# Kernel tuning notes

Hardware: AMD Instinct MI355X
Metric: run time of the kernel (lower is better)

## Reference

```python
import jax, jax.numpy as jnp
import numpy as np

N, E, B = 65536, 262144, 2048   # nodes, edges, graphs
ND, ED, H, L = 32, 8, 128, 4    # node feat, edge feat, hidden, egnn layers
PE, PH, CH = 1280, 512, 512     # protein embed, protein hidden, combined hidden
EPS = 1e-8


def _seg_mean(data, ids, num):
    s = jax.ops.segment_sum(data, ids, num_segments=num)
    c = jax.ops.segment_sum(jnp.ones((data.shape[0], 1), data.dtype), ids, num_segments=num)
    return s / jnp.clip(c, 1.0)


def setup_inputs() -> dict:
    key = jax.random.key(0)
    ks = iter(jax.random.split(key, 40))

    def p(shape, scale=0.05):
        return jax.random.normal(next(ks), shape, dtype=jnp.float32) * scale

    inp = {
        "x": jax.random.normal(next(ks), (N, ND), dtype=jnp.float32),
        "pos": jax.random.normal(next(ks), (N, 3), dtype=jnp.float32),
        "edge_attr": jax.random.uniform(next(ks), (E, ED), dtype=jnp.float32),
        "protein_embedding": jax.random.normal(next(ks), (B, PE), dtype=jnp.float32),
        "edge_index": jax.random.randint(next(ks), (2, E), 0, N),
        "batch": jnp.arange(N, dtype=jnp.int64) // (N // B),
        # EGNN embeddings
        "emb_in_w": p((ND, H)), "emb_in_b": p((H,)),
        "emb_out_w": p((H, H)), "emb_out_b": p((H,)),
        # per-layer stacked params (leading dim L)
        "edge_w1": p((L, 2 * H + 1 + ED, H)), "edge_b1": p((L, H)),
        "edge_w2": p((L, H, H)), "edge_b2": p((L, H)),
        "att_w": p((L, H, 1)), "att_b": p((L, 1)),
        "coord_w1": p((L, H, H)), "coord_b1": p((L, H)),
        "coord_w2": p((L, H, 1)),  # no bias, xavier in torch impl
        "node_w1": p((L, 2 * H, H)), "node_b1": p((L, H)),
        "node_w2": p((L, H, H)), "node_b2": p((L, H)),
        # protein + combined heads
        "prot_w": p((PE, PH)), "prot_b": p((PH,)),
        "comb_w1": p((H + PH, CH)), "comb_b1": p((CH,)),
        "comb_w2": p((CH, 1)), "comb_b2": p((1,)),
    }
    return inp


def _forward(x, pos, edge_attr, protein_embedding,
             emb_in_w, emb_in_b, emb_out_w, emb_out_b,
             edge_w1, edge_b1, edge_w2, edge_b2, att_w, att_b,
             coord_w1, coord_b1, coord_w2,
             node_w1, node_b1, node_w2, node_b2,
             prot_w, prot_b, comb_w1, comb_b1, comb_w2, comb_b2,
             edge_index, batch):
    row, col = edge_index[0], edge_index[1]
    h = x @ emb_in_w + emb_in_b
    for l in range(L):
        # coord2radial (normalize=True)
        d = pos[row] - pos[col]                       # [E,3]
        radial = jnp.sum(d * d, axis=-1, keepdims=True)  # [E,1]
        d = d / (jnp.sqrt(radial) + EPS)
        # edge model with sigmoid attention gate
        e_in = jnp.concatenate([h[row], h[col], radial, edge_attr], axis=-1)
        m = jax.nn.silu(e_in @ edge_w1[l] + edge_b1[l])
        m = jax.nn.silu(m @ edge_w2[l] + edge_b2[l])
        m = m * jax.nn.sigmoid(m @ att_w[l] + att_b[l])
        # coord model (tanh=True, coords_agg='mean')
        t = jax.nn.silu(m @ coord_w1[l] + coord_b1[l])
        trans = d * jnp.tanh(t @ coord_w2[l])         # [E,3]
        pos = pos + _seg_mean(trans, row, N)
        # node model (sum aggregation, residual)
        agg = jax.ops.segment_sum(m, row, num_segments=N)
        nh = jax.nn.silu(jnp.concatenate([h, agg], axis=-1) @ node_w1[l] + node_b1[l])
        h = h + (nh @ node_w2[l] + node_b2[l])
    h = h @ emb_out_w + emb_out_b
    # global mean pool over graphs
    drug = _seg_mean(h, batch, B)                     # [B,H]
    prot = jax.nn.relu(protein_embedding @ prot_w + prot_b)  # dropout = identity (eval)
    c = jnp.concatenate([drug, prot], axis=-1)
    c = jax.nn.relu(c @ comb_w1 + comb_b1)
    logits = (c @ comb_w2 + comb_b2)[:, 0]
    return logits


def reference(x, pos, edge_attr, protein_embedding,
              emb_in_w, emb_in_b, emb_out_w, emb_out_b,
              edge_w1, edge_b1, edge_w2, edge_b2, att_w, att_b,
              coord_w1, coord_b1, coord_w2,
              node_w1, node_b1, node_w2, node_b2,
              prot_w, prot_b, comb_w1, comb_b1, comb_w2, comb_b2,
              edge_index, batch):
    logits = _forward(x, pos, edge_attr, protein_embedding,
                      emb_in_w, emb_in_b, emb_out_w, emb_out_b,
                      edge_w1, edge_b1, edge_w2, edge_b2, att_w, att_b,
                      coord_w1, coord_b1, coord_w2,
                      node_w1, node_b1, node_w2, node_b2,
                      prot_w, prot_b, comb_w1, comb_b1, comb_w2, comb_b2,
                      edge_index, batch)
    attention_weights = jnp.zeros((B, 1, 1), dtype=logits.dtype)
    return logits, attention_weights
```

## Files before the change

kernel.cpp:

```cpp
#include <hip/hip_runtime.h>
#include <math.h>


static constexpr int NN  = 65536;
static constexpr int NE  = 262144;
static constexpr int NB  = 2048;
static constexpr int NDF = 32;
static constexpr int HD  = 128;
static constexpr int NL  = 4;
static constexpr int PED = 1280;
static constexpr int PHD = 512;
static constexpr int CHD = 512;
static constexpr float EPSV = 1e-8f;

static constexpr int KK1 = 9;
static constexpr int KK2 = 4;
static constexpr int KKN1 = 8;
static constexpr int KKP = 40;
static constexpr int KKC = 20;

static constexpr int ES = 36;

typedef __attribute__((ext_vector_type(8))) short bf8_t;
typedef __attribute__((ext_vector_type(4))) float f4_t;

__device__ __forceinline__ float sigmoid_f(float x) {
  return __fdividef(1.0f, 1.0f + __expf(-x));
}
__device__ __forceinline__ float silu_f(float x) { return x * sigmoid_f(x); }

__device__ __forceinline__ ushort f2bf(float f) {
  unsigned u = __float_as_uint(f);
  u += 0x7FFFu + ((u >> 16) & 1u);
  return (ushort)(u >> 16);
}
__device__ __forceinline__ float bf2f(ushort h) {
  return __uint_as_float(((unsigned)h) << 16);
}
__device__ __forceinline__ unsigned pk2bf(float a, float b) {
  unsigned r;
  asm("v_cvt_pk_bf16_f32 %0, %1, %2" : "=v"(r) : "v"(a), "v"(b));
  return r;
}

__device__ __forceinline__ void fma44(float (&acc)[4][4], const float4 a, const float4 w) {
  const float av[4] = {a.x, a.y, a.z, a.w};
  const float wv[4] = {w.x, w.y, w.z, w.w};
#pragma unroll
  for (int i = 0; i < 4; ++i)
#pragma unroll
    for (int j = 0; j < 4; ++j) acc[i][j] = fmaf(av[i], wv[j], acc[i][j]);
}


__global__ void hist_kernel(const int* __restrict__ ei, int* __restrict__ deg) {
  const int e = blockIdx.x * 256 + threadIdx.x;
  if (e < NE) atomicAdd(&deg[ei[e]], 1);
}

__global__ __launch_bounds__(256) void scan1_kernel(const int* __restrict__ deg,
                                                    int* __restrict__ cbase) {
  __shared__ int wsum[4];
  const int t = threadIdx.x;
  const int lane = t & 63, wave = t >> 6;
  int s = 0;
  const int4* p = (const int4*)deg + (size_t)t * 64;
#pragma unroll 8
  for (int j = 0; j < 64; ++j) {
    const int4 v = p[j];
    s += v.x + v.y + v.z + v.w;
  }
  int incl = s;
#pragma unroll
  for (int d = 1; d < 64; d <<= 1) {
    const int u = __shfl_up(incl, d, 64);
    if (lane >= d) incl += u;
  }
  if (lane == 63) wsum[wave] = incl;
  __syncthreads();
  int base = 0;
  for (int w2 = 0; w2 < wave; ++w2) base += wsum[w2];
  cbase[t] = base + incl - s;
}

__global__ __launch_bounds__(256) void scan2_kernel(const int* __restrict__ deg,
                                                    const int* __restrict__ cbase,
                                                    int* __restrict__ row_ptr) {
  __shared__ int wsum[4];
  const int b = blockIdx.x, t = threadIdx.x;
  const int lane = t & 63, wave = t >> 6;
  const int i = b * 256 + t;
  const int s = deg[i];
  int incl = s;
#pragma unroll
  for (int d = 1; d < 64; d <<= 1) {
    const int u = __shfl_up(incl, d, 64);
    if (lane >= d) incl += u;
  }
  if (lane == 63) wsum[wave] = incl;
  __syncthreads();
  int base = cbase[b];
  for (int w2 = 0; w2 < wave; ++w2) base += wsum[w2];
  row_ptr[i + 1] = base + incl;
  if (i == 0) row_ptr[0] = 0;
}

__global__ void fill_kernel(const int* __restrict__ ei, const int* __restrict__ row_ptr,
                            int* __restrict__ fill_pos, int* __restrict__ edge_ids) {
  const int e = blockIdx.x * 256 + threadIdx.x;
  if (e < NE) {
    const int n = ei[e];
    const int s = atomicAdd(&fill_pos[n], 1);
    edge_ids[row_ptr[n] + s] = e;
  }
}

__global__ void perm_kernel(const int* __restrict__ ei, const int* __restrict__ edge_ids,
                            const float* __restrict__ edge_attr,
                            int* __restrict__ rowp, int* __restrict__ colp,
                            ushort* __restrict__ extra) {
  const int i = blockIdx.x * 256 + threadIdx.x;
  if (i >= NE) return;
  const int e = edge_ids[i];
  rowp[i] = ei[e];
  colp[i] = ei[NE + e];
  const float4 a = *(const float4*)(edge_attr + (size_t)e * 8);
  const float4 b = *(const float4*)(edge_attr + (size_t)e * 8 + 4);
  ushort* dst = extra + (size_t)i * 32;
  *(uint4*)(dst) = make_uint4(pk2bf(0.0f, a.x), pk2bf(a.y, a.z),
                              pk2bf(a.w, b.x), pk2bf(b.y, b.z));
  *(uint4*)(dst + 8)  = make_uint4(pk2bf(b.w, 0.0f), 0, 0, 0);
  *(uint4*)(dst + 16) = make_uint4(0, 0, 0, 0);
  *(uint4*)(dst + 24) = make_uint4(0, 0, 0, 0);
}

__global__ void pos_copy_kernel(const float* __restrict__ pos, float* __restrict__ pc) {
  const int n = blockIdx.x * 256 + threadIdx.x;
  if (n < NN) {
    const float4 v = make_float4(pos[(size_t)n * 3 + 0], pos[(size_t)n * 3 + 1],
                                 pos[(size_t)n * 3 + 2], 0.0f);
    *(float4*)(pc + (size_t)n * 4) = v;
  }
}


__global__ __launch_bounds__(256) void packw_kernel(
    const float* __restrict__ W, ushort* __restrict__ Wp,
    int K, int N, int KK, size_t sW, size_t sWp) {
  const int layer = blockIdx.y;
  const int NTG = N >> 4;
  const int i = blockIdx.x * 256 + threadIdx.x;
  if (i >= KK * NTG * 64) return;
  const int l = i & 63;
  const int q = i >> 6;
  const int ntg = q % NTG;
  const int kk = q / NTG;
  const int k0 = kk * 32 + ((l >> 4) * 8);
  const int n = ntg * 16 + (l & 15);
  const float* w = W + layer * sW;
  unsigned ww[4];
#pragma unroll
  for (int p = 0; p < 4; ++p) {
    const int ka = k0 + p * 2, kb = ka + 1;
    const unsigned lo = (ka < K) ? f2bf(w[(size_t)ka * N + n]) : 0;
    const unsigned hi = (kb < K) ? f2bf(w[(size_t)kb * N + n]) : 0;
    ww[p] = lo | (hi << 16);
  }
  *(uint4*)(Wp + layer * sWp + (size_t)i * 8) = make_uint4(ww[0], ww[1], ww[2], ww[3]);
}

__global__ __launch_bounds__(256) void cvt_bf_kernel(const float* __restrict__ in,
                                                     ushort* __restrict__ out, int n) {
  const int i = blockIdx.x * 256 + threadIdx.x;
  if (i * 8 >= n) return;
  const float4 v0 = *(const float4*)(in + (size_t)i * 8);
  const float4 v1 = *(const float4*)(in + (size_t)i * 8 + 4);
  *(uint4*)(out + (size_t)i * 8) =
      make_uint4(pk2bf(v0.x, v0.y), pk2bf(v0.z, v0.w), pk2bf(v1.x, v1.y), pk2bf(v1.z, v1.w));
}


__global__ __launch_bounds__(256) void geom_kernel(
    const float* __restrict__ pos_cur,
    const int* __restrict__ rowp, const int* __restrict__ colp,
    float* __restrict__ dnb, ushort* __restrict__ extra) {
  const int i = blockIdx.x * 256 + threadIdx.x;
  if (i >= NE) return;
  const int r = rowp[i], c = colp[i];
  const float4 pr = *(const float4*)(pos_cur + (size_t)r * 4);
  const float4 pc = *(const float4*)(pos_cur + (size_t)c * 4);
  const float dx = pr.x - pc.x, dy = pr.y - pc.y, dz = pr.z - pc.z;
  const float radial = dx * dx + dy * dy + dz * dz;
  const float inv = 1.0f / (sqrtf(radial) + EPSV);
  *(float4*)(dnb + (size_t)i * 4) = make_float4(dx * inv, dy * inv, dz * inv, 0.0f);
  extra[(size_t)i * 32] = f2bf(radial);
}


__global__ __launch_bounds__(256) void emb_in_kernel(
    const float* __restrict__ x, const float* __restrict__ W,
    const float* __restrict__ B, float* __restrict__ h, ushort* __restrict__ hbf) {
  __shared__ float xs[NDF * ES];
  const int t = threadIdx.x;
  const int n0 = blockIdx.x * 32;
  {
    const int r = t >> 3;
    const int kq = (t & 7) * 4;
    const float4 v = *(const float4*)(x + (size_t)(n0 + r) * NDF + kq);
    xs[(kq + 0) * ES + r] = v.x;
    xs[(kq + 1) * ES + r] = v.y;
    xs[(kq + 2) * ES + r] = v.z;
    xs[(kq + 3) * ES + r] = v.w;
  }
  __syncthreads();
  const int eg = t & 7, fg = t >> 3;
  float acc[4][4] = {};
  const float* wp = W + fg * 4;
#pragma unroll
  for (int k = 0; k < NDF; ++k) {
    const float4 a = *(const float4*)&xs[k * ES + eg * 4];
    const float4 w = *(const float4*)(wp + (size_t)k * HD);
    fma44(acc, a, w);
  }
  const float4 bv = *(const float4*)(B + fg * 4);
  const float bb[4] = {bv.x, bv.y, bv.z, bv.w};
#pragma unroll
  for (int i = 0; i < 4; ++i) {
    const float4 o = make_float4(acc[i][0] + bb[0], acc[i][1] + bb[1],
                                 acc[i][2] + bb[2], acc[i][3] + bb[3]);
    *(float4*)(h + (size_t)(n0 + eg * 4 + i) * HD + fg * 4) = o;
    *(uint2*)(hbf + (size_t)(n0 + eg * 4 + i) * HD + fg * 4) =
        make_uint2(pk2bf(o.x, o.y), pk2bf(o.z, o.w));
  }
}


__global__ __launch_bounds__(256) void edge_mfma_kernel(
    const ushort* __restrict__ hbf, const ushort* __restrict__ extra,
    const int* __restrict__ rowp, const int* __restrict__ colp,
    const float* __restrict__ dnb,
    const ushort* __restrict__ W1p, const float* __restrict__ B1,
    const ushort* __restrict__ W2p, const float* __restrict__ B2,
    const float* __restrict__ AW, const float* __restrict__ AB,
    const ushort* __restrict__ CW1p, const float* __restrict__ CB1,
    const float* __restrict__ CW2,
    ushort* __restrict__ m_bf, float* __restrict__ trans_out) {
  __shared__ ushort mtileT[64 * 128];
  __shared__ int ridx[64], cidx[64];
  __shared__ float redbuf[2][64];
  __shared__ float gates[64];

  const int t = threadIdx.x;
  const int bid = blockIdx.x;
  const int e0 = ((bid & 7) * (NE / 64 / 8) + (bid >> 3)) * 64;
  if (t < 64) {
    ridx[t] = rowp[e0 + t];
    cidx[t] = colp[e0 + t];
  }
  __syncthreads();

  const int w = t >> 6, l = t & 63;
  const int wn = w & 1, we = w >> 1;
  const int g = l >> 4, ln = l & 15;
  const int nb = wn * 64;
  const int eb = we * 32;

  int je[2], er[2], ec[2], swz[2];
#pragma unroll
  for (int et = 0; et < 2; ++et) {
    je[et] = eb + et * 16 + ln;
    er[et] = ridx[je[et]];
    ec[et] = cidx[je[et]];
    swz[et] = (je[et] & 7) << 3;
  }

  const f4_t zf = {0.0f, 0.0f, 0.0f, 0.0f};
  f4_t acc[4][2];
#pragma unroll
  for (int mt = 0; mt < 4; ++mt)
#pragma unroll
    for (int et = 0; et < 2; ++et) acc[mt][et] = zf;

#pragma unroll
  for (int kk = 0; kk < KK1; ++kk) {
    bf8_t aw[4], be[2];
#pragma unroll
    for (int mt = 0; mt < 4; ++mt)
      aw[mt] = *(const bf8_t*)(W1p + ((size_t)(kk * 8 + wn * 4 + mt) * 64 + l) * 8);
#pragma unroll
    for (int et = 0; et < 2; ++et) {
      if (kk < 8) {
        const int idx = (kk < 4) ? er[et] : ec[et];
        be[et] = *(const bf8_t*)(hbf + (size_t)idx * HD + (kk & 3) * 32 + g * 8);
      } else {
        be[et] = *(const bf8_t*)(extra + (size_t)(e0 + je[et]) * 32 + g * 8);
      }
    }
#pragma unroll
    for (int mt = 0; mt < 4; ++mt)
#pragma unroll
      for (int et = 0; et < 2; ++et)
        acc[mt][et] = __builtin_amdgcn_mfma_f32_16x16x32_bf16(aw[mt], be[et], acc[mt][et], 0, 0, 0);
  }

#pragma unroll
  for (int mt = 0; mt < 4; ++mt) {
    const int n0 = nb + mt * 16 + g * 4;
    const float4 bv = *(const float4*)(B1 + n0);
#pragma unroll
    for (int et = 0; et < 2; ++et) {
      const unsigned lo = pk2bf(silu_f(acc[mt][et][0] + bv.x), silu_f(acc[mt][et][1] + bv.y));
      const unsigned hi = pk2bf(silu_f(acc[mt][et][2] + bv.z), silu_f(acc[mt][et][3] + bv.w));
      *(uint2*)&mtileT[je[et] * HD + (n0 ^ swz[et])] = make_uint2(lo, hi);
    }
  }
  __syncthreads();

  f4_t acc2[4][2];
#pragma unroll
  for (int mt = 0; mt < 4; ++mt)
#pragma unroll
    for (int et = 0; et < 2; ++et) acc2[mt][et] = zf;
#pragma unroll
  for (int kk = 0; kk < KK2; ++kk) {
    bf8_t aw[4], be[2];
#pragma unroll
    for (int mt = 0; mt < 4; ++mt)
      aw[mt] = *(const bf8_t*)(W2p + ((size_t)(kk * 8 + wn * 4 + mt) * 64 + l) * 8);
    const int nk = kk * 32 + g * 8;
#pragma unroll
    for (int et = 0; et < 2; ++et)
      be[et] = *(const bf8_t*)&mtileT[je[et] * HD + (nk ^ swz[et])];
#pragma unroll
    for (int mt = 0; mt < 4; ++mt)
#pragma unroll
      for (int et = 0; et < 2; ++et)
        acc2[mt][et] = __builtin_amdgcn_mfma_f32_16x16x32_bf16(aw[mt], be[et], acc2[mt][et], 0, 0, 0);
  }

  float m2v[4][2][4];
  {
    float p[2] = {0.0f, 0.0f};
#pragma unroll
    for (int mt = 0; mt < 4; ++mt) {
      const int n0 = nb + mt * 16 + g * 4;
      const float4 bv = *(const float4*)(B2 + n0);
      const float4 av = *(const float4*)(AW + n0);
      const float bb[4] = {bv.x, bv.y, bv.z, bv.w};
      const float aa[4] = {av.x, av.y, av.z, av.w};
#pragma unroll
      for (int et = 0; et < 2; ++et)
#pragma unroll
        for (int r = 0; r < 4; ++r) {
          const float v = silu_f(acc2[mt][et][r] + bb[r]);
          m2v[mt][et][r] = v;
          p[et] = fmaf(v, aa[r], p[et]);
        }
    }
#pragma unroll
    for (int et = 0; et < 2; ++et) {
      p[et] += __shfl_xor(p[et], 16, 64);
      p[et] += __shfl_xor(p[et], 32, 64);
    }
    if (l < 16) {
#pragma unroll
      for (int et = 0; et < 2; ++et) redbuf[wn][eb + et * 16 + l] = p[et];
    }
  }
  __syncthreads();
  if (t < 64) gates[t] = sigmoid_f(redbuf[0][t] + redbuf[1][t] + AB[0]);
  __syncthreads();

  {
    float grow[2];
#pragma unroll
    for (int et = 0; et < 2; ++et) grow[et] = gates[je[et]];
#pragma unroll
    for (int mt = 0; mt < 4; ++mt) {
      const int n0 = nb + mt * 16 + g * 4;
#pragma unroll
      for (int et = 0; et < 2; ++et) {
        const unsigned lo = pk2bf(m2v[mt][et][0] * grow[et], m2v[mt][et][1] * grow[et]);
        const unsigned hi = pk2bf(m2v[mt][et][2] * grow[et], m2v[mt][et][3] * grow[et]);
        *(uint2*)&mtileT[je[et] * HD + (n0 ^ swz[et])] = make_uint2(lo, hi);
      }
    }
  }
  __syncthreads();

  f4_t acc3[4][2];
#pragma unroll
  for (int mt = 0; mt < 4; ++mt)
#pragma unroll
    for (int et = 0; et < 2; ++et) acc3[mt][et] = zf;
#pragma unroll
  for (int kk = 0; kk < KK2; ++kk) {
    bf8_t aw[4], be[2];
#pragma unroll
    for (int mt = 0; mt < 4; ++mt)
      aw[mt] = *(const bf8_t*)(CW1p + ((size_t)(kk * 8 + wn * 4 + mt) * 64 + l) * 8);
    const int nk = kk * 32 + g * 8;
#pragma unroll
    for (int et = 0; et < 2; ++et)
      be[et] = *(const bf8_t*)&mtileT[je[et] * HD + (nk ^ swz[et])];
#pragma unroll
    for (int mt = 0; mt < 4; ++mt)
#pragma unroll
      for (int et = 0; et < 2; ++et)
        acc3[mt][et] = __builtin_amdgcn_mfma_f32_16x16x32_bf16(aw[mt], be[et], acc3[mt][et], 0, 0, 0);
  }
  {
    float q[2] = {0.0f, 0.0f};
#pragma unroll
    for (int mt = 0; mt < 4; ++mt) {
      const int n0 = nb + mt * 16 + g * 4;
      const float4 bv = *(const float4*)(CB1 + n0);
      const float4 cv = *(const float4*)(CW2 + n0);
      const float bb[4] = {bv.x, bv.y, bv.z, bv.w};
      const float cc[4] = {cv.x, cv.y, cv.z, cv.w};
#pragma unroll
      for (int et = 0; et < 2; ++et)
#pragma unroll
        for (int r = 0; r < 4; ++r)
          q[et] = fmaf(silu_f(acc3[mt][et][r] + bb[r]), cc[r], q[et]);
    }
#pragma unroll
    for (int et = 0; et < 2; ++et) {
      q[et] += __shfl_xor(q[et], 16, 64);
      q[et] += __shfl_xor(q[et], 32, 64);
    }
    if (l < 16) {
#pragma unroll
      for (int et = 0; et < 2; ++et) redbuf[wn][eb + et * 16 + l] = q[et];
    }
  }
  __syncthreads();
  if (t < 64) {
    const float s = tanhf(redbuf[0][t] + redbuf[1][t]);
    const f4_t dn = *(const f4_t*)(dnb + (size_t)(e0 + t) * 4);
    const f4_t tr = dn * s;
    *(f4_t*)(trans_out + (size_t)(e0 + t) * 4) = tr;
  }

#pragma unroll
  for (int it = 0; it < 4; ++it) {
    const int i = it * 256 + t;
    const int row = i >> 4;
    const int c8 = (i & 15) * 8;
    const uint4 v = *(const uint4*)&mtileT[row * HD + (c8 ^ ((row & 7) << 3))];
    *(uint4*)(m_bf + (size_t)(e0 + row) * HD + c8) = v;
  }
}


__global__ __launch_bounds__(256) void gather_kernel(
    const ushort* __restrict__ m_bf, const float* __restrict__ trans,
    const int* __restrict__ row_ptr,
    ushort* __restrict__ agg_bf, float* __restrict__ pos_cur) {
  const int t = threadIdx.x;
  const int wave = t >> 6, lane = t & 63;
  const int n = blockIdx.x * 4 + wave;
  const int s = row_ptr[n], e_end = row_ptr[n + 1];
  float a0 = 0.0f, a1 = 0.0f, ta = 0.0f;
  for (int i = s; i < e_end; ++i) {
    const ushort2 v = *(const ushort2*)(m_bf + (size_t)i * HD + lane * 2);
    a0 += bf2f(v.x);
    a1 += bf2f(v.y);
    if (lane < 4) ta += trans[(size_t)i * 4 + lane];
  }
  *(unsigned*)(agg_bf + (size_t)n * HD + lane * 2) = pk2bf(a0, a1);
  if (lane < 3) {
    const int dg = e_end - s;
    pos_cur[(size_t)n * 4 + lane] += ta / (float)(dg > 0 ? dg : 1);
  }
}


__global__ __launch_bounds__(256) void node_mfma_kernel(
    float* __restrict__ h, const ushort* __restrict__ hbf,
    const ushort* __restrict__ agg_bf,
    const ushort* __restrict__ W1p, const float* __restrict__ B1,
    const ushort* __restrict__ W2p, const float* __restrict__ B2,
    ushort* __restrict__ hbf_out) {
  __shared__ ushort mtileT[64 * 128];
  const int t = threadIdx.x;
  const int n0blk = blockIdx.x * 64;
  const int w = t >> 6, l = t & 63;
  const int wn = w & 1, we = w >> 1;
  const int g = l >> 4, ln = l & 15;
  const int nb = wn * 64;
  const int eb = we * 32;

  int jn[2], swz[2];
#pragma unroll
  for (int et = 0; et < 2; ++et) {
    jn[et] = eb + et * 16 + ln;
    swz[et] = (jn[et] & 7) << 3;
  }

  const f4_t zf = {0.0f, 0.0f, 0.0f, 0.0f};
  f4_t acc[4][2];
#pragma unroll
  for (int mt = 0; mt < 4; ++mt)
#pragma unroll
    for (int et = 0; et < 2; ++et) acc[mt][et] = zf;

#pragma unroll
  for (int kk = 0; kk < KKN1; ++kk) {
    bf8_t aw[4], be[2];
#pragma unroll
    for (int mt = 0; mt < 4; ++mt)
      aw[mt] = *(const bf8_t*)(W1p + ((size_t)(kk * 8 + wn * 4 + mt) * 64 + l) * 8);
#pragma unroll
    for (int et = 0; et < 2; ++et) {
      const size_t base = (size_t)(n0blk + jn[et]) * HD + (kk & 3) * 32 + g * 8;
      be[et] = (kk < 4) ? *(const bf8_t*)(hbf + base) : *(const bf8_t*)(agg_bf + base);
    }
#pragma unroll
    for (int mt = 0; mt < 4; ++mt)
#pragma unroll
      for (int et = 0; et < 2; ++et)
        acc[mt][et] = __builtin_amdgcn_mfma_f32_16x16x32_bf16(aw[mt], be[et], acc[mt][et], 0, 0, 0);
  }
#pragma unroll
  for (int mt = 0; mt < 4; ++mt) {
    const int n0 = nb + mt * 16 + g * 4;
    const float4 bv = *(const float4*)(B1 + n0);
#pragma unroll
    for (int et = 0; et < 2; ++et) {
      const unsigned lo = pk2bf(silu_f(acc[mt][et][0] + bv.x), silu_f(acc[mt][et][1] + bv.y));
      const unsigned hi = pk2bf(silu_f(acc[mt][et][2] + bv.z), silu_f(acc[mt][et][3] + bv.w));
      *(uint2*)&mtileT[jn[et] * HD + (n0 ^ swz[et])] = make_uint2(lo, hi);
    }
  }
  __syncthreads();

  f4_t acc2[4][2];
#pragma unroll
  for (int mt = 0; mt < 4; ++mt)
#pragma unroll
    for (int et = 0; et < 2; ++et) acc2[mt][et] = zf;
#pragma unroll
  for (int kk = 0; kk < KK2; ++kk) {
    bf8_t aw[4], be[2];
#pragma unroll
    for (int mt = 0; mt < 4; ++mt)
      aw[mt] = *(const bf8_t*)(W2p + ((size_t)(kk * 8 + wn * 4 + mt) * 64 + l) * 8);
    const int nk = kk * 32 + g * 8;
#pragma unroll
    for (int et = 0; et < 2; ++et)
      be[et] = *(const bf8_t*)&mtileT[jn[et] * HD + (nk ^ swz[et])];
#pragma unroll
    for (int mt = 0; mt < 4; ++mt)
#pragma unroll
      for (int et = 0; et < 2; ++et)
        acc2[mt][et] = __builtin_amdgcn_mfma_f32_16x16x32_bf16(aw[mt], be[et], acc2[mt][et], 0, 0, 0);
  }
#pragma unroll
  for (int mt = 0; mt < 4; ++mt) {
    const int n0 = nb + mt * 16 + g * 4;
    const float4 bv = *(const float4*)(B2 + n0);
#pragma unroll
    for (int et = 0; et < 2; ++et) {
      float* hp = h + (size_t)(n0blk + jn[et]) * HD + n0;
      const float4 old = *(const float4*)hp;
      float4 o;
      o.x = old.x + acc2[mt][et][0] + bv.x;
      o.y = old.y + acc2[mt][et][1] + bv.y;
      o.z = old.z + acc2[mt][et][2] + bv.z;
      o.w = old.w + acc2[mt][et][3] + bv.w;
      *(float4*)hp = o;
      *(uint2*)(hbf_out + (size_t)(n0blk + jn[et]) * HD + n0) =
          make_uint2(pk2bf(o.x, o.y), pk2bf(o.z, o.w));
    }
  }
}


__global__ __launch_bounds__(256) void gemm_head_kernel(
    const ushort* __restrict__ A, const ushort* __restrict__ Wp,
    const float* __restrict__ bias, ushort* __restrict__ out,
    int lda, int KK, int NTG, int ldo, int col_off) {
  const int t = threadIdx.x;
  const int rb = blockIdx.x * 64;
  const int cb = blockIdx.y * 128;
  const int w = t >> 6, l = t & 63;
  const int wr = w >> 1, wc = w & 1;
  const int g = l >> 4, ln = l & 15;
  const int row0 = wr * 32;
  int rowA[2];
#pragma unroll
  for (int mt = 0; mt < 2; ++mt) rowA[mt] = row0 + mt * 16 + ln;

  const f4_t zf = {0.0f, 0.0f, 0.0f, 0.0f};
  f4_t acc[2][4];
#pragma unroll
  for (int mt = 0; mt < 2; ++mt)
#pragma unroll
    for (int nt = 0; nt < 4; ++nt) acc[mt][nt] = zf;

  const int ntg0 = (cb >> 4) + wc * 4;
  for (int kk = 0; kk < KK; ++kk) {
    bf8_t a[2], b[4];
#pragma unroll
    for (int mt = 0; mt < 2; ++mt)
      a[mt] = *(const bf8_t*)(A + (size_t)(rb + rowA[mt]) * lda + kk * 32 + g * 8);
#pragma unroll
    for (int nt = 0; nt < 4; ++nt)
      b[nt] = *(const bf8_t*)(Wp + ((size_t)(kk * NTG + ntg0 + nt) * 64 + l) * 8);
#pragma unroll
    for (int mt = 0; mt < 2; ++mt)
#pragma unroll
      for (int nt = 0; nt < 4; ++nt)
        acc[mt][nt] = __builtin_amdgcn_mfma_f32_16x16x32_bf16(a[mt], b[nt], acc[mt][nt], 0, 0, 0);
  }
  {
    float bn[4];
#pragma unroll
    for (int nt = 0; nt < 4; ++nt) bn[nt] = bias[cb + wc * 64 + nt * 16 + ln];
#pragma unroll
    for (int mt = 0; mt < 2; ++mt)
#pragma unroll
      for (int nt = 0; nt < 4; ++nt) {
        const int col = cb + wc * 64 + nt * 16 + ln;
#pragma unroll
        for (int r = 0; r < 4; ++r) {
          const int row = row0 + mt * 16 + g * 4 + r;
          const float v = fmaxf(acc[mt][nt][r] + bn[nt], 0.0f);
          out[(size_t)(rb + row) * ldo + col_off + col] = f2bf(v);
        }
      }
  }
}


__global__ __launch_bounds__(128) void pool_kernel(
    const float* __restrict__ h, const float* __restrict__ W,
    const float* __restrict__ B, ushort* __restrict__ c_in) {
  __shared__ float mh[HD];
  const int g = blockIdx.x, t = threadIdx.x;
  float s = 0.0f;
#pragma unroll 4
  for (int n = 0; n < 32; ++n) s += h[((size_t)g * 32 + n) * HD + t];
  mh[t] = s * (1.0f / 32.0f);
  __syncthreads();
  float acc = B[t];
#pragma unroll 4
  for (int k = 0; k < HD; ++k) acc = fmaf(mh[k], W[(size_t)k * HD + t], acc);
  c_in[(size_t)g * (HD + PHD) + t] = f2bf(acc);
}

__global__ __launch_bounds__(256) void logits_kernel(
    const ushort* __restrict__ c, const float* __restrict__ w2,
    const float* __restrict__ b2, float* __restrict__ out) {
  const int t = threadIdx.x;
  const int wave = t >> 6, lane = t & 63;
  const int r = blockIdx.x * 4 + wave;
  const ushort* cp = c + (size_t)r * CHD + lane * 8;
  const float* wp = w2 + lane * 8;
  float s = 0.0f;
#pragma unroll
  for (int j = 0; j < 8; ++j) s = fmaf(bf2f(cp[j]), wp[j], s);
#pragma unroll
  for (int off = 32; off > 0; off >>= 1) s += __shfl_down(s, off, 64);
  if (lane == 0) {
    out[r] = s + b2[0];
    out[NB + r] = 0.0f;
  }
}


extern "C" void kernel_launch(void* const* d_in, const int* in_sizes, int n_in,
                              void* d_out, int out_size, void* d_ws, size_t ws_size,
                              hipStream_t stream) {
  const float* x          = (const float*)d_in[0];
  const float* pos        = (const float*)d_in[1];
  const float* edge_attr  = (const float*)d_in[2];
  const float* pe         = (const float*)d_in[3];
  const int*   edge_index = (const int*)d_in[4];
  const float* emb_in_w   = (const float*)d_in[6];
  const float* emb_in_b   = (const float*)d_in[7];
  const float* emb_out_w  = (const float*)d_in[8];
  const float* emb_out_b  = (const float*)d_in[9];
  const float* edge_w1    = (const float*)d_in[10];
  const float* edge_b1    = (const float*)d_in[11];
  const float* edge_w2    = (const float*)d_in[12];
  const float* edge_b2    = (const float*)d_in[13];
  const float* att_w      = (const float*)d_in[14];
  const float* att_b      = (const float*)d_in[15];
  const float* coord_w1   = (const float*)d_in[16];
  const float* coord_b1   = (const float*)d_in[17];
  const float* coord_w2   = (const float*)d_in[18];
  const float* node_w1    = (const float*)d_in[19];
  const float* node_b1    = (const float*)d_in[20];
  const float* node_w2    = (const float*)d_in[21];
  const float* node_b2    = (const float*)d_in[22];
  const float* prot_w     = (const float*)d_in[23];
  const float* prot_b     = (const float*)d_in[24];
  const float* comb_w1    = (const float*)d_in[25];
  const float* comb_b1    = (const float*)d_in[26];
  const float* comb_w2    = (const float*)d_in[27];
  const float* comb_b2    = (const float*)d_in[28];
  float* out = (float*)d_out;
  (void)in_sizes; (void)n_in; (void)out_size; (void)ws_size;

  char* ws = (char*)d_ws;
  size_t off = 0;
  auto carve = [&](size_t bytes) -> void* {
    void* p = ws + off;
    off += (bytes + 255) & ~(size_t)255;
    return p;
  };
  float*  h       = (float*)carve((size_t)NN * HD * 4);
  ushort* h_bf    = (ushort*)carve((size_t)NN * HD * 2);
  ushort* agg_bf  = (ushort*)carve((size_t)NN * HD * 2);
  ushort* m_bf    = (ushort*)carve((size_t)NE * HD * 2);
  float*  trans   = (float*)carve((size_t)NE * 4 * 4);
  float*  dnb     = (float*)carve((size_t)NE * 4 * 4);
  ushort* extra   = (ushort*)carve((size_t)NE * 32 * 2);
  float*  pos_cur = (float*)carve((size_t)NN * 4 * 4);
  ushort* pe_bf   = (ushort*)carve((size_t)NB * PED * 2);
  ushort* c_in    = (ushort*)carve((size_t)NB * (HD + PHD) * 2);
  ushort* c1      = (ushort*)carve((size_t)NB * CHD * 2);
  const size_t sW1p  = (size_t)KK1 * 8 * 64 * 8;
  const size_t sW2p  = (size_t)KK2 * 8 * 64 * 8;
  const size_t sNW1p = (size_t)KKN1 * 8 * 64 * 8;
  const size_t sPWp  = (size_t)KKP * 32 * 64 * 8;
  const size_t sCWp  = (size_t)KKC * 32 * 64 * 8;
  ushort* W1p     = (ushort*)carve(sW1p * NL * 2);
  ushort* W2p     = (ushort*)carve(sW2p * NL * 2);
  ushort* CW1p    = (ushort*)carve(sW2p * NL * 2);
  ushort* NW1p    = (ushort*)carve(sNW1p * NL * 2);
  ushort* NW2p    = (ushort*)carve(sW2p * NL * 2);
  ushort* PWp     = (ushort*)carve(sPWp * 2);
  ushort* CWp     = (ushort*)carve(sCWp * 2);
  int* deg        = (int*)carve((size_t)NN * 4);
  int* row_ptr    = (int*)carve((size_t)(NN + 1) * 4);
  int* fill_pos   = (int*)carve((size_t)NN * 4);
  int* edge_ids   = (int*)carve((size_t)NE * 4);
  int* rowp       = (int*)carve((size_t)NE * 4);
  int* colp       = (int*)carve((size_t)NE * 4);
  int* cbase      = (int*)carve((size_t)256 * 4);

  hipMemsetAsync(deg, 0, (size_t)NN * 4, stream);
  hipMemsetAsync(fill_pos, 0, (size_t)NN * 4, stream);

  pos_copy_kernel<<<NN / 256, 256, 0, stream>>>(pos, pos_cur);
  hist_kernel<<<NE / 256, 256, 0, stream>>>(edge_index, deg);
  scan1_kernel<<<1, 256, 0, stream>>>(deg, cbase);
  scan2_kernel<<<NN / 256, 256, 0, stream>>>(deg, cbase, row_ptr);
  fill_kernel<<<NE / 256, 256, 0, stream>>>(edge_index, row_ptr, fill_pos, edge_ids);
  perm_kernel<<<NE / 256, 256, 0, stream>>>(edge_index, edge_ids, edge_attr,
                                            rowp, colp, extra);

  packw_kernel<<<dim3(18, NL), 256, 0, stream>>>(edge_w1, W1p, 265, HD, KK1,
                                                 (size_t)265 * HD, sW1p);
  packw_kernel<<<dim3(8, NL), 256, 0, stream>>>(edge_w2, W2p, HD, HD, KK2,
                                                (size_t)HD * HD, sW2p);
  packw_kernel<<<dim3(8, NL), 256, 0, stream>>>(coord_w1, CW1p, HD, HD, KK2,
                                                (size_t)HD * HD, sW2p);
  packw_kernel<<<dim3(16, NL), 256, 0, stream>>>(node_w1, NW1p, 2 * HD, HD, KKN1,
                                                 (size_t)2 * HD * HD, sNW1p);
  packw_kernel<<<dim3(8, NL), 256, 0, stream>>>(node_w2, NW2p, HD, HD, KK2,
                                                (size_t)HD * HD, sW2p);
  packw_kernel<<<dim3(320, 1), 256, 0, stream>>>(prot_w, PWp, PED, PHD, KKP, 0, 0);
  packw_kernel<<<dim3(160, 1), 256, 0, stream>>>(comb_w1, CWp, HD + PHD, CHD, KKC, 0, 0);

  cvt_bf_kernel<<<NB * PED / (256 * 8), 256, 0, stream>>>(pe, pe_bf, NB * PED);

  emb_in_kernel<<<NN / 32, 256, 0, stream>>>(x, emb_in_w, emb_in_b, h, h_bf);

  for (int l = 0; l < NL; ++l) {
    geom_kernel<<<NE / 256, 256, 0, stream>>>(pos_cur, rowp, colp, dnb, extra);
    edge_mfma_kernel<<<NE / 64, 256, 0, stream>>>(
        h_bf, extra, rowp, colp, dnb,
        W1p + (size_t)l * sW1p, edge_b1 + (size_t)l * HD,
        W2p + (size_t)l * sW2p, edge_b2 + (size_t)l * HD,
        att_w + (size_t)l * HD, att_b + l,
        CW1p + (size_t)l * sW2p, coord_b1 + (size_t)l * HD,
        coord_w2 + (size_t)l * HD,
        m_bf, trans);
    gather_kernel<<<NN / 4, 256, 0, stream>>>(m_bf, trans, row_ptr, agg_bf, pos_cur);
    node_mfma_kernel<<<NN / 64, 256, 0, stream>>>(
        h, h_bf, agg_bf,
        NW1p + (size_t)l * sNW1p, node_b1 + (size_t)l * HD,
        NW2p + (size_t)l * sW2p, node_b2 + (size_t)l * HD, h_bf);
  }

  pool_kernel<<<NB, 128, 0, stream>>>(h, emb_out_w, emb_out_b, c_in);
  gemm_head_kernel<<<dim3(NB / 64, PHD / 128), 256, 0, stream>>>(
      pe_bf, PWp, prot_b, c_in, PED, KKP, PHD / 16, HD + PHD, HD);
  gemm_head_kernel<<<dim3(NB / 64, CHD / 128), 256, 0, stream>>>(
      c_in, CWp, comb_b1, c1, HD + PHD, KKC, CHD / 16, CHD, 0);
  logits_kernel<<<NB / 4, 256, 0, stream>>>(c1, comb_w2, comb_b2, out);
}
```

Measured before the change: 966.4 us.

## Fuse edge geometry computation into edge MFMA kernel and drop dnb buffer

Removes the separate geom_kernel launch per layer and computes relative positions, radial distance and normalized direction inside edge_mfma_kernel, keeping them in LDS. The radial value is patched into the extra bf16 operand in registers instead of being written to global memory, and the dnb global buffer is dropped. The kernel also recomputes silu on acc2 instead of holding an m2v register array and adds a launch_bounds occupancy hint of 8 to reduce register pressure. Costs are recomputing silu and a possible register spill under the tighter bound.

New measurement: 1.183 ms. 22.5% more time.

```diff
diff --git a/kernel.cpp b/kernel.cpp
--- a/kernel.cpp
+++ b/kernel.cpp
@@ -180,23 +180,6 @@
 }
 
 
-__global__ __launch_bounds__(256) void geom_kernel(
-    const float* __restrict__ pos_cur,
-    const int* __restrict__ rowp, const int* __restrict__ colp,
-    float* __restrict__ dnb, ushort* __restrict__ extra) {
-  const int i = blockIdx.x * 256 + threadIdx.x;
-  if (i >= NE) return;
-  const int r = rowp[i], c = colp[i];
-  const float4 pr = *(const float4*)(pos_cur + (size_t)r * 4);
-  const float4 pc = *(const float4*)(pos_cur + (size_t)c * 4);
-  const float dx = pr.x - pc.x, dy = pr.y - pc.y, dz = pr.z - pc.z;
-  const float radial = dx * dx + dy * dy + dz * dz;
-  const float inv = 1.0f / (sqrtf(radial) + EPSV);
-  *(float4*)(dnb + (size_t)i * 4) = make_float4(dx * inv, dy * inv, dz * inv, 0.0f);
-  extra[(size_t)i * 32] = f2bf(radial);
-}
-
-
 __global__ __launch_bounds__(256) void emb_in_kernel(
     const float* __restrict__ x, const float* __restrict__ W,
     const float* __restrict__ B, float* __restrict__ h, ushort* __restrict__ hbf) {
@@ -235,10 +218,10 @@
 }
 
 
-__global__ __launch_bounds__(256) void edge_mfma_kernel(
+__global__ __launch_bounds__(256, 8) void edge_mfma_kernel(
     const ushort* __restrict__ hbf, const ushort* __restrict__ extra,
     const int* __restrict__ rowp, const int* __restrict__ colp,
-    const float* __restrict__ dnb,
+    const float* __restrict__ pos_cur,
     const ushort* __restrict__ W1p, const float* __restrict__ B1,
     const ushort* __restrict__ W2p, const float* __restrict__ B2,
     const float* __restrict__ AW, const float* __restrict__ AB,
@@ -249,13 +232,24 @@
   __shared__ int ridx[64], cidx[64];
   __shared__ float redbuf[2][64];
   __shared__ float gates[64];
+  __shared__ float dnb_lds[64 * 4];
+  __shared__ ushort rad_lds[64];
 
   const int t = threadIdx.x;
   const int bid = blockIdx.x;
   const int e0 = ((bid & 7) * (NE / 64 / 8) + (bid >> 3)) * 64;
   if (t < 64) {
-    ridx[t] = rowp[e0 + t];
-    cidx[t] = colp[e0 + t];
+    const int r = rowp[e0 + t];
+    const int c = colp[e0 + t];
+    ridx[t] = r;
+    cidx[t] = c;
+    const float4 pr = *(const float4*)(pos_cur + (size_t)r * 4);
+    const float4 pc = *(const float4*)(pos_cur + (size_t)c * 4);
+    const float dx = pr.x - pc.x, dy = pr.y - pc.y, dz = pr.z - pc.z;
+    const float radial = dx * dx + dy * dy + dz * dz;
+    const float inv = 1.0f / (sqrtf(radial) + EPSV);
+    *(float4*)(dnb_lds + t * 4) = make_float4(dx * inv, dy * inv, dz * inv, 0.0f);
+    rad_lds[t] = f2bf(radial);
   }
   __syncthreads();
 
@@ -294,6 +288,8 @@
         be[et] = *(const bf8_t*)(hbf + (size_t)idx * HD + (kk & 3) * 32 + g * 8);
       } else {
         be[et] = *(const bf8_t*)(extra + (size_t)(e0 + je[et]) * 32 + g * 8);
+        const short rad = (short)rad_lds[je[et]];
+        if (g == 0) be[et][0] = rad;
       }
     }
 #pragma unroll
@@ -338,7 +334,6 @@
         acc2[mt][et] = __builtin_amdgcn_mfma_f32_16x16x32_bf16(aw[mt], be[et], acc2[mt][et], 0, 0, 0);
   }
 
-  float m2v[4][2][4];
   {
     float p[2] = {0.0f, 0.0f};
 #pragma unroll
@@ -351,11 +346,8 @@
 #pragma unroll
       for (int et = 0; et < 2; ++et)
 #pragma unroll
-        for (int r = 0; r < 4; ++r) {
-          const float v = silu_f(acc2[mt][et][r] + bb[r]);
-          m2v[mt][et][r] = v;
-          p[et] = fmaf(v, aa[r], p[et]);
-        }
+        for (int r = 0; r < 4; ++r)
+          p[et] = fmaf(silu_f(acc2[mt][et][r] + bb[r]), aa[r], p[et]);
     }
 #pragma unroll
     for (int et = 0; et < 2; ++et) {
@@ -371,19 +363,18 @@
   if (t < 64) gates[t] = sigmoid_f(redbuf[0][t] + redbuf[1][t] + AB[0]);
   __syncthreads();
 
-  {
-    float grow[2];
-#pragma unroll
-    for (int et = 0; et < 2; ++et) grow[et] = gates[je[et]];
-#pragma unroll
-    for (int mt = 0; mt < 4; ++mt) {
-      const int n0 = nb + mt * 16 + g * 4;
-#pragma unroll
-      for (int et = 0; et < 2; ++et) {
-        const unsigned lo = pk2bf(m2v[mt][et][0] * grow[et], m2v[mt][et][1] * grow[et]);
-        const unsigned hi = pk2bf(m2v[mt][et][2] * grow[et], m2v[mt][et][3] * grow[et]);
-        *(uint2*)&mtileT[je[et] * HD + (n0 ^ swz[et])] = make_uint2(lo, hi);
-      }
+#pragma unroll
+  for (int mt = 0; mt < 4; ++mt) {
+    const int n0 = nb + mt * 16 + g * 4;
+    const float4 bv = *(const float4*)(B2 + n0);
+#pragma unroll
+    for (int et = 0; et < 2; ++et) {
+      const float gr = gates[je[et]];
+      const unsigned lo = pk2bf(silu_f(acc2[mt][et][0] + bv.x) * gr,
+                                silu_f(acc2[mt][et][1] + bv.y) * gr);
+      const unsigned hi = pk2bf(silu_f(acc2[mt][et][2] + bv.z) * gr,
+                                silu_f(acc2[mt][et][3] + bv.w) * gr);
+      *(uint2*)&mtileT[je[et] * HD + (n0 ^ swz[et])] = make_uint2(lo, hi);
     }
   }
   __syncthreads();
@@ -437,9 +428,9 @@
   __syncthreads();
   if (t < 64) {
     const float s = tanhf(redbuf[0][t] + redbuf[1][t]);
-    const f4_t dn = *(const f4_t*)(dnb + (size_t)(e0 + t) * 4);
-    const f4_t tr = dn * s;
-    *(f4_t*)(trans_out + (size_t)(e0 + t) * 4) = tr;
+    const float4 dn = *(const float4*)(dnb_lds + t * 4);
+    *(float4*)(trans_out + (size_t)(e0 + t) * 4) =
+        make_float4(dn.x * s, dn.y * s, dn.z * s, 0.0f);
   }
 
 #pragma unroll
@@ -716,7 +707,6 @@
   ushort* agg_bf  = (ushort*)carve((size_t)NN * HD * 2);
   ushort* m_bf    = (ushort*)carve((size_t)NE * HD * 2);
   float*  trans   = (float*)carve((size_t)NE * 4 * 4);
-  float*  dnb     = (float*)carve((size_t)NE * 4 * 4);
   ushort* extra   = (ushort*)carve((size_t)NE * 32 * 2);
   float*  pos_cur = (float*)carve((size_t)NN * 4 * 4);
   ushort* pe_bf   = (ushort*)carve((size_t)NB * PED * 2);
@@ -771,9 +761,8 @@
   emb_in_kernel<<<NN / 32, 256, 0, stream>>>(x, emb_in_w, emb_in_b, h, h_bf);
 
   for (int l = 0; l < NL; ++l) {
-    geom_kernel<<<NE / 256, 256, 0, stream>>>(pos_cur, rowp, colp, dnb, extra);
     edge_mfma_kernel<<<NE / 64, 256, 0, stream>>>(
-        h_bf, extra, rowp, colp, dnb,
+        h_bf, extra, rowp, colp, pos_cur,
         W1p + (size_t)l * sW1p, edge_b1 + (size_t)l * HD,
         W2p + (size_t)l * sW2p, edge_b2 + (size_t)l * HD,
         att_w + (size_t)l * HD, att_b + l,
```
